# Performance work log

Hardware: AMD Instinct MI355X
Metric: run time of the kernel (lower is better)

The kernel has to match this reference:

```python
import jax, jax.numpy as jnp
import numpy as np

EMBED = 1024
HEADS = 16
DK = EMBED // HEADS


def setup_inputs() -> dict:
    key = jax.random.key(0)
    ks = jax.random.split(key, 6)
    B, S = 2, 2048
    scale = 1.0 / np.sqrt(EMBED)
    x = jax.random.normal(ks[0], (B, S, EMBED), dtype=jnp.float32)
    Wq = jax.random.normal(ks[1], (EMBED, EMBED), dtype=jnp.float32) * scale
    Wk = jax.random.normal(ks[2], (EMBED, EMBED), dtype=jnp.float32) * scale
    Wv = jax.random.normal(ks[3], (EMBED, EMBED), dtype=jnp.float32) * scale
    Wo = jax.random.normal(ks[4], (EMBED, EMBED), dtype=jnp.float32) * scale
    qw = jnp.zeros((HEADS, 1), dtype=jnp.float32)  # quantum_weight, init quantum_scale=0
    return {"x": x, "Wq": Wq, "Wk": Wk, "Wv": Wv, "Wo": Wo, "qw": qw}


def reference(x, Wq, Wk, Wv, Wo, qw):
    B, S, E = x.shape
    # nn.Linear with no bias: y = x @ W.T; split heads -> [B,H,S,Dk]
    def proj(W):
        return (x @ W.T).reshape(B, S, HEADS, DK).transpose(0, 2, 1, 3)
    q, k, v = proj(Wq), proj(Wk), proj(Wv)
    scores = jnp.einsum('bhsd,bhtd->bhst', q, k) / np.sqrt(DK)
    attn = jax.nn.softmax(scores, axis=-1)  # dropout in eval mode: identity
    classical = jnp.einsum('bhst,bhtd->bhsd', attn, v)
    w = jax.nn.sigmoid(qw)[:, :, None]  # [H,1,1] per-head mixing weight
    out = w * jnp.sin(classical) + (1.0 - w) * classical
    out = out.transpose(0, 2, 1, 3).reshape(B, S, E)
    return out @ Wo.T
```

## Files before the change

### kernel.cpp

```cpp
#include <hip/hip_runtime.h>
#include <math.h>

constexpr int Ec  = 1024;
constexpr int Hc  = 16;
constexpr int DKc = 64;
constexpr int Bc  = 2;
constexpr int Sc  = 2048;
constexpr int Mc  = Bc * Sc;

typedef _Float16 half8 __attribute__((ext_vector_type(8)));
typedef _Float16 half4 __attribute__((ext_vector_type(4)));
typedef float    floatx4 __attribute__((ext_vector_type(4)));

#define MFMA16(a, b, c) __builtin_amdgcn_mfma_f32_16x16x32_f16(a, b, c, 0, 0, 0)

__device__ __forceinline__ void async_lds16(const _Float16* g, _Float16* l)
{
    __builtin_amdgcn_global_load_lds(
        (const __attribute__((address_space(1))) unsigned int*)g,
        (__attribute__((address_space(3))) unsigned int*)l, 16, 0, 0);
}

__global__ __launch_bounds__(256)
void convert_to_h(const float4* __restrict__ x,
                  const float4* __restrict__ wq,
                  const float4* __restrict__ wk,
                  const float4* __restrict__ wv,
                  const float4* __restrict__ wo,
                  half4* __restrict__ dst)
{
    const int i = blockIdx.x * 256 + threadIdx.x;
    const float4* src; int off;
    if      (i < 1048576) { src = x;  off = i; }
    else if (i < 1310720) { src = wq; off = i - 1048576; }
    else if (i < 1572864) { src = wk; off = i - 1310720; }
    else if (i < 1835008) { src = wv; off = i - 1572864; }
    else                  { src = wo; off = i - 1835008; }
    const float4 v = src[off];
    half4 o;
    o.x = (_Float16)v.x; o.y = (_Float16)v.y;
    o.z = (_Float16)v.z; o.w = (_Float16)v.w;
    dst[i] = o;
}

__device__ __forceinline__ void mfma_gemm_core64(const _Float16* __restrict__ A,
                                                 const _Float16* __restrict__ Bw,
                                                 int m0, int n0,
                                                 _Float16* As, _Float16* Bs,
                                                 floatx4 acc[4][4])
{
    const int tid  = threadIdx.x;
    const int wave = tid >> 6, lane = tid & 63;
    const int l16  = lane & 15, quad = lane >> 4;
    const int wrow = (wave >> 1) * 64, wcol = (wave & 1) * 64;

    const int srow8  = lane >> 3;
    const int schunk = (lane & 7) ^ (srow8 & 7);
    const _Float16* ga = A  + (size_t)(m0 + wave * 32 + srow8) * Ec + schunk * 8;
    const _Float16* gb = Bw + (size_t)(n0 + wave * 32 + srow8) * Ec + schunk * 8;
    _Float16* lA = As + (size_t)(wave * 32) * 64;
    _Float16* lB = Bs + (size_t)(wave * 32) * 64;

    for (int kt = 0; kt < Ec; kt += 64) {
#pragma unroll
        for (int c = 0; c < 4; ++c) {
            async_lds16(ga + (size_t)(c * 8) * Ec + kt, lA + c * 512);
            async_lds16(gb + (size_t)(c * 8) * Ec + kt, lB + c * 512);
        }
        __syncthreads();

        half8 af[4][2], bf[4][2];
#pragma unroll
        for (int i = 0; i < 4; ++i) {
            const int ra = wrow + i * 16 + l16;
            const int rb = wcol + i * 16 + l16;
#pragma unroll
            for (int kc = 0; kc < 2; ++kc) {
                af[i][kc] = *(const half8*)&As[ra * 64 + (((quad + kc * 4) ^ (ra & 7)) * 8)];
                bf[i][kc] = *(const half8*)&Bs[rb * 64 + (((quad + kc * 4) ^ (rb & 7)) * 8)];
            }
        }
#pragma unroll
        for (int i = 0; i < 4; ++i)
#pragma unroll
            for (int j = 0; j < 4; ++j) {
                acc[i][j] = MFMA16(af[i][0], bf[j][0], acc[i][j]);
                acc[i][j] = MFMA16(af[i][1], bf[j][1], acc[i][j]);
            }
        __syncthreads();
    }
}

__global__ __launch_bounds__(256)
void gemm_qkv_mfma(const _Float16* __restrict__ xh,
                   const _Float16* __restrict__ wqh,
                   const _Float16* __restrict__ wkh,
                   const _Float16* __restrict__ wvh,
                   _Float16* __restrict__ Qh,
                   _Float16* __restrict__ Kh,
                   _Float16* __restrict__ VTh)
{
    __shared__ __align__(16) _Float16 As[128 * 64];
    __shared__ __align__(16) _Float16 Bs[128 * 64];
    const int z = blockIdx.z;
    const _Float16* W = (z == 0) ? wqh : (z == 1) ? wkh : wvh;
    const int m0 = blockIdx.y * 128, n0 = blockIdx.x * 128;

    floatx4 acc[4][4] = {};
    mfma_gemm_core64(xh, W, m0, n0, As, Bs, acc);

    const int tid  = threadIdx.x;
    const int wave = tid >> 6, lane = tid & 63;
    const int l16  = lane & 15, quad = lane >> 4;
    const int wrow = (wave >> 1) * 64, wcol = (wave & 1) * 64;

    if (z == 2) {
#pragma unroll
        for (int i = 0; i < 4; ++i)
#pragma unroll
            for (int j = 0; j < 4; ++j) {
                const int n  = n0 + wcol + j * 16 + l16;
                const int hh = n >> 6, d = n & 63;
                const int mb = m0 + wrow + i * 16 + quad * 4;
                const int bb = mb >> 11, s = mb & (Sc - 1);
                half4 pk;
#pragma unroll
                for (int r = 0; r < 4; ++r) pk[r] = (_Float16)acc[i][j][r];
                *(half4*)&VTh[((size_t)((bb * Hc + hh) * DKc + d)) * Sc + s] = pk;
            }
    } else {
        _Float16* out = (z == 0) ? Qh : Kh;
        const float scale = (z == 0) ? 0.125f : 1.0f;
#pragma unroll
        for (int i = 0; i < 4; ++i)
#pragma unroll
            for (int j = 0; j < 4; ++j) {
                const int n = n0 + wcol + j * 16 + l16;
#pragma unroll
                for (int r = 0; r < 4; ++r) {
                    const int m = m0 + wrow + i * 16 + quad * 4 + r;
                    out[(size_t)m * Ec + n] = (_Float16)(acc[i][j][r] * scale);
                }
            }
    }
}

__global__ __launch_bounds__(256)
void gemm_out_mfma(const _Float16* __restrict__ A,
                   const _Float16* __restrict__ W,
                   float* __restrict__ C)
{
    __shared__ __align__(16) _Float16 As[128 * 64];
    __shared__ __align__(16) _Float16 Bs[64 * 64];
    const int m0 = blockIdx.y * 128, n0 = blockIdx.x * 64;

    const int tid  = threadIdx.x;
    const int wave = tid >> 6, lane = tid & 63;
    const int l16  = lane & 15, quad = lane >> 4;
    const int wrow = (wave >> 1) * 64, wcol = (wave & 1) * 32;

    const int srow8  = lane >> 3;
    const int schunk = (lane & 7) ^ (srow8 & 7);
    const _Float16* ga = A + (size_t)(m0 + wave * 32 + srow8) * Ec + schunk * 8;
    const _Float16* gb = W + (size_t)(n0 + wave * 16 + srow8) * Ec + schunk * 8;
    _Float16* lA = As + (size_t)(wave * 32) * 64;
    _Float16* lB = Bs + (size_t)(wave * 16) * 64;

    floatx4 acc[4][2] = {};

    for (int kt = 0; kt < Ec; kt += 64) {
#pragma unroll
        for (int c = 0; c < 4; ++c)
            async_lds16(ga + (size_t)(c * 8) * Ec + kt, lA + c * 512);
#pragma unroll
        for (int c = 0; c < 2; ++c)
            async_lds16(gb + (size_t)(c * 8) * Ec + kt, lB + c * 512);
        __syncthreads();

        half8 af[4][2], bf[2][2];
#pragma unroll
        for (int i = 0; i < 4; ++i) {
            const int ra = wrow + i * 16 + l16;
#pragma unroll
            for (int kc = 0; kc < 2; ++kc)
                af[i][kc] = *(const half8*)&As[ra * 64 + (((quad + kc * 4) ^ (ra & 7)) * 8)];
        }
#pragma unroll
        for (int j = 0; j < 2; ++j) {
            const int rb = wcol + j * 16 + l16;
#pragma unroll
            for (int kc = 0; kc < 2; ++kc)
                bf[j][kc] = *(const half8*)&Bs[rb * 64 + (((quad + kc * 4) ^ (rb & 7)) * 8)];
        }
#pragma unroll
        for (int i = 0; i < 4; ++i)
#pragma unroll
            for (int j = 0; j < 2; ++j) {
                acc[i][j] = MFMA16(af[i][0], bf[j][0], acc[i][j]);
                acc[i][j] = MFMA16(af[i][1], bf[j][1], acc[i][j]);
            }
        __syncthreads();
    }

#pragma unroll
    for (int i = 0; i < 4; ++i)
#pragma unroll
        for (int j = 0; j < 2; ++j) {
            const int n = n0 + wcol + j * 16 + l16;
#pragma unroll
            for (int r = 0; r < 4; ++r) {
                const int m = m0 + wrow + i * 16 + quad * 4 + r;
                C[(size_t)m * Ec + n] = acc[i][j][r];
            }
        }
}

__global__ __launch_bounds__(256)
void flash_attn(const _Float16* __restrict__ Qh,
                const _Float16* __restrict__ Kh,
                const _Float16* __restrict__ VTh,
                const float* __restrict__ qw,
                _Float16* __restrict__ Mixh)
{
    constexpr int BM = 128, BN = 64, LDH = 72;
    __shared__ _Float16 Kt[BN][LDH];
    __shared__ _Float16 Vt[DKc][LDH];
    __shared__ _Float16 Ps[BM][LDH];

    const int tid  = threadIdx.x;
    const int wave = tid >> 6, lane = tid & 63;
    const int quad = lane >> 4, l16 = lane & 15;
    const int q0 = blockIdx.x * BM;
    const int bh = blockIdx.y;
    const int h  = bh & (Hc - 1), b = bh >> 4;

    half8 aq[2][2];
#pragma unroll
    for (int u = 0; u < 2; ++u) {
        const _Float16* qp = Qh + (size_t)(b * Sc + q0 + wave * 32 + u * 16 + l16) * Ec
                                + h * DKc + quad * 8;
        aq[u][0] = *(const half8*)qp;
        aq[u][1] = *(const half8*)(qp + 32);
    }

    const int srow = tid >> 2;
    const int sseg = (tid & 3) * 16;
    const _Float16* Kg = Kh + (size_t)(b * Sc + srow) * Ec + h * DKc + sseg;
    const _Float16* Vg = VTh + ((size_t)(bh * DKc + srow)) * Sc + sseg;

    half8 kr0 = *(const half8*)Kg, kr1 = *(const half8*)(Kg + 8);
    half8 vr0 = *(const half8*)Vg, vr1 = *(const half8*)(Vg + 8);
    Kg += (size_t)BN * Ec; Vg += BN;
    *(half8*)&Kt[srow][sseg]     = kr0;
    *(half8*)&Kt[srow][sseg + 8] = kr1;

    floatx4 o[2][4] = {};
    float l_run[2] = {0.f, 0.f};

    for (int n = 0; n < Sc / BN; ++n) {
        __syncthreads();
        *(half8*)&Vt[srow][sseg]     = vr0;
        *(half8*)&Vt[srow][sseg + 8] = vr1;
        const bool more = (n + 1 < Sc / BN);
        if (more) {
            kr0 = *(const half8*)Kg; kr1 = *(const half8*)(Kg + 8);
            vr0 = *(const half8*)Vg; vr1 = *(const half8*)(Vg + 8);
            Kg += (size_t)BN * Ec; Vg += BN;
        }

        floatx4 st[2][4];
#pragma unroll
        for (int i = 0; i < 4; ++i) {
            const half8 ak0 = *(const half8*)&Kt[i * 16 + l16][quad * 8];
            const half8 ak1 = *(const half8*)&Kt[i * 16 + l16][32 + quad * 8];
            const floatx4 z = {0.f, 0.f, 0.f, 0.f};
            st[0][i] = MFMA16(ak1, aq[0][1], MFMA16(ak0, aq[0][0], z));
            st[1][i] = MFMA16(ak1, aq[1][1], MFMA16(ak0, aq[1][0], z));
        }

#pragma unroll
        for (int u = 0; u < 2; ++u) {
            const int prow = wave * 32 + u * 16 + l16;
#pragma unroll
            for (int i = 0; i < 4; ++i) {
                const float p0 = __expf(st[u][i][0]);
                const float p1 = __expf(st[u][i][1]);
                const float p2 = __expf(st[u][i][2]);
                const float p3 = __expf(st[u][i][3]);
                l_run[u] += (p0 + p1) + (p2 + p3);
                half4 pk;
                pk.x = (_Float16)p0; pk.y = (_Float16)p1;
                pk.z = (_Float16)p2; pk.w = (_Float16)p3;
                *(half4*)&Ps[prow][i * 16 + quad * 4] = pk;
            }
        }
        __syncthreads();

        half8 ap[2][2];
#pragma unroll
        for (int u = 0; u < 2; ++u) {
            const _Float16* pp = &Ps[wave * 32 + u * 16 + l16][quad * 8];
            ap[u][0] = *(const half8*)pp;
            ap[u][1] = *(const half8*)(pp + 32);
        }
#pragma unroll
        for (int jd = 0; jd < 4; ++jd) {
            const half8 bv0 = *(const half8*)&Vt[jd * 16 + l16][quad * 8];
            const half8 bv1 = *(const half8*)&Vt[jd * 16 + l16][32 + quad * 8];
#pragma unroll
            for (int u = 0; u < 2; ++u) {
                o[u][jd] = MFMA16(ap[u][0], bv0, o[u][jd]);
                o[u][jd] = MFMA16(ap[u][1], bv1, o[u][jd]);
            }
        }

        if (more) {
            *(half8*)&Kt[srow][sseg]     = kr0;
            *(half8*)&Kt[srow][sseg + 8] = kr1;
        }
    }

    const float wmix = 1.f / (1.f + __expf(-qw[h]));
#pragma unroll
    for (int u = 0; u < 2; ++u) {
        l_run[u] += __shfl_xor(l_run[u], 16);
        l_run[u] += __shfl_xor(l_run[u], 32);
    }
#pragma unroll
    for (int u = 0; u < 2; ++u)
#pragma unroll
        for (int r = 0; r < 4; ++r) {
            const float l = __shfl(l_run[u], (lane & 48) | (quad * 4 + r));
            const float inv = 1.f / l;
            const int m = q0 + wave * 32 + u * 16 + quad * 4 + r;
            _Float16* mp = Mixh + (size_t)(b * Sc + m) * Ec + h * DKc;
#pragma unroll
            for (int jd = 0; jd < 4; ++jd) {
                const float v = o[u][jd][r] * inv;
                mp[jd * 16 + l16] = (_Float16)(wmix * __sinf(v) + (1.f - wmix) * v);
            }
        }
}

extern "C" void kernel_launch(void* const* d_in, const int* in_sizes, int n_in,
                              void* d_out, int out_size, void* d_ws, size_t ws_size,
                              hipStream_t stream)
{
    const float* x  = (const float*)d_in[0];
    const float* Wq = (const float*)d_in[1];
    const float* Wk = (const float*)d_in[2];
    const float* Wv = (const float*)d_in[3];
    const float* Wo = (const float*)d_in[4];
    const float* qw = (const float*)d_in[5];
    float* out = (float*)d_out;

    _Float16* hb   = (_Float16*)d_ws;
    _Float16* xh   = hb;
    _Float16* wqh  = hb + (size_t)4 * 1024 * 1024;
    _Float16* wkh  = hb + (size_t)5 * 1024 * 1024;
    _Float16* wvh  = hb + (size_t)6 * 1024 * 1024;
    _Float16* woh  = hb + (size_t)7 * 1024 * 1024;
    _Float16* Qh   = hb + (size_t)8 * 1024 * 1024;
    _Float16* Kh   = hb + (size_t)12 * 1024 * 1024;
    _Float16* VTh  = hb + (size_t)16 * 1024 * 1024;
    _Float16* mixh = hb + (size_t)20 * 1024 * 1024;

    convert_to_h<<<dim3(8192), dim3(256), 0, stream>>>(
        (const float4*)x, (const float4*)Wq, (const float4*)Wk,
        (const float4*)Wv, (const float4*)Wo, (half4*)hb);

    gemm_qkv_mfma<<<dim3(Ec / 128, Mc / 128, 3), dim3(256), 0, stream>>>(
        xh, wqh, wkh, wvh, Qh, Kh, VTh);

    flash_attn<<<dim3(Sc / 128, Bc * Hc), dim3(256), 0, stream>>>(
        Qh, Kh, VTh, qw, mixh);

    gemm_out_mfma<<<dim3(Ec / 64, Mc / 128), dim3(256), 0, stream>>>(
        mixh, woh, out);
}
```

Measured before the change: 194.9 us.

## Split flash attention KV sequence across two wave groups and merge in LDS

Doubles the flash attention block to 512 threads, with each half of the block processing half of the key/value sequence for the same query tile. Partial sums and output accumulators are combined through shared memory at the end. It also folds log2(e) into the Q scale so the kernel can use the native exp2, and packs P to fp16 with cvt_pkrtz. This raises per-block parallelism and latency hiding, at the cost of more LDS, an extra reduction step, and round-toward-zero fp16 conversion.

```diff
diff --git a/kernel.cpp b/kernel.cpp
--- a/kernel.cpp
+++ b/kernel.cpp
@@ -130,7 +130,7 @@
             }
     } else {
         _Float16* out = (z == 0) ? Qh : Kh;
-        const float scale = (z == 0) ? 0.125f : 1.0f;
+        const float scale = (z == 0) ? 0.18033688011112042f : 1.0f;
 #pragma unroll
         for (int i = 0; i < 4; ++i)
 #pragma unroll
@@ -215,7 +215,7 @@
         }
 }
 
-__global__ __launch_bounds__(256)
+__global__ __launch_bounds__(512)
 void flash_attn(const _Float16* __restrict__ Qh,
                 const _Float16* __restrict__ Kh,
                 const _Float16* __restrict__ VTh,
@@ -223,30 +223,38 @@
                 _Float16* __restrict__ Mixh)
 {
     constexpr int BM = 128, BN = 64, LDH = 72;
-    __shared__ _Float16 Kt[BN][LDH];
-    __shared__ _Float16 Vt[DKc][LDH];
-    __shared__ _Float16 Ps[BM][LDH];
+    constexpr int NT = (Sc / BN) / 2;
+    __shared__ __align__(16) _Float16 KVs[2][2][BN][LDH];
+    __shared__ __align__(16) _Float16 Ps[2][BM][LDH];
+    __shared__ float Ls[BM];
 
     const int tid  = threadIdx.x;
-    const int wave = tid >> 6, lane = tid & 63;
+    const int g    = tid >> 8;
+    const int wl   = (tid >> 6) & 3;
+    const int lane = tid & 63;
     const int quad = lane >> 4, l16 = lane & 15;
     const int q0 = blockIdx.x * BM;
     const int bh = blockIdx.y;
     const int h  = bh & (Hc - 1), b = bh >> 4;
 
+    _Float16 (*Kt)[LDH] = KVs[g][0];
+    _Float16 (*Vt)[LDH] = KVs[g][1];
+    _Float16 (*Pt)[LDH] = Ps[g];
+
     half8 aq[2][2];
 #pragma unroll
     for (int u = 0; u < 2; ++u) {
-        const _Float16* qp = Qh + (size_t)(b * Sc + q0 + wave * 32 + u * 16 + l16) * Ec
+        const _Float16* qp = Qh + (size_t)(b * Sc + q0 + wl * 32 + u * 16 + l16) * Ec
                                 + h * DKc + quad * 8;
         aq[u][0] = *(const half8*)qp;
         aq[u][1] = *(const half8*)(qp + 32);
     }
 
-    const int srow = tid >> 2;
-    const int sseg = (tid & 3) * 16;
-    const _Float16* Kg = Kh + (size_t)(b * Sc + srow) * Ec + h * DKc + sseg;
-    const _Float16* Vg = VTh + ((size_t)(bh * DKc + srow)) * Sc + sseg;
+    const int tl   = tid & 255;
+    const int srow = tl >> 2;
+    const int sseg = (tl & 3) * 16;
+    const _Float16* Kg = Kh + (size_t)(b * Sc + g * (Sc / 2) + srow) * Ec + h * DKc + sseg;
+    const _Float16* Vg = VTh + ((size_t)(bh * DKc + srow)) * Sc + g * (Sc / 2) + sseg;
 
     half8 kr0 = *(const half8*)Kg, kr1 = *(const half8*)(Kg + 8);
     half8 vr0 = *(const half8*)Vg, vr1 = *(const half8*)(Vg + 8);
@@ -257,11 +265,11 @@
     floatx4 o[2][4] = {};
     float l_run[2] = {0.f, 0.f};
 
-    for (int n = 0; n < Sc / BN; ++n) {
+    for (int n = 0; n < NT; ++n) {
         __syncthreads();
         *(half8*)&Vt[srow][sseg]     = vr0;
         *(half8*)&Vt[srow][sseg + 8] = vr1;
-        const bool more = (n + 1 < Sc / BN);
+        const bool more = (n + 1 < NT);
         if (more) {
             kr0 = *(const half8*)Kg; kr1 = *(const half8*)(Kg + 8);
             vr0 = *(const half8*)Vg; vr1 = *(const half8*)(Vg + 8);
@@ -280,18 +288,20 @@
 
 #pragma unroll
         for (int u = 0; u < 2; ++u) {
-            const int prow = wave * 32 + u * 16 + l16;
+            const int prow = wl * 32 + u * 16 + l16;
 #pragma unroll
             for (int i = 0; i < 4; ++i) {
-                const float p0 = __expf(st[u][i][0]);
-                const float p1 = __expf(st[u][i][1]);
-                const float p2 = __expf(st[u][i][2]);
-                const float p3 = __expf(st[u][i][3]);
+                const float p0 = __builtin_amdgcn_exp2f(st[u][i][0]);
+                const float p1 = __builtin_amdgcn_exp2f(st[u][i][1]);
+                const float p2 = __builtin_amdgcn_exp2f(st[u][i][2]);
+                const float p3 = __builtin_amdgcn_exp2f(st[u][i][3]);
                 l_run[u] += (p0 + p1) + (p2 + p3);
+                auto lo = __builtin_amdgcn_cvt_pkrtz(p0, p1);
+                auto hi = __builtin_amdgcn_cvt_pkrtz(p2, p3);
                 half4 pk;
-                pk.x = (_Float16)p0; pk.y = (_Float16)p1;
-                pk.z = (_Float16)p2; pk.w = (_Float16)p3;
-                *(half4*)&Ps[prow][i * 16 + quad * 4] = pk;
+                pk.x = (_Float16)lo.x; pk.y = (_Float16)lo.y;
+                pk.z = (_Float16)hi.x; pk.w = (_Float16)hi.y;
+                *(half4*)&Pt[prow][i * 16 + quad * 4] = pk;
             }
         }
         __syncthreads();
@@ -299,7 +309,7 @@
         half8 ap[2][2];
 #pragma unroll
         for (int u = 0; u < 2; ++u) {
-            const _Float16* pp = &Ps[wave * 32 + u * 16 + l16][quad * 8];
+            const _Float16* pp = &Pt[wl * 32 + u * 16 + l16][quad * 8];
             ap[u][0] = *(const half8*)pp;
             ap[u][1] = *(const half8*)(pp + 32);
         }
@@ -320,26 +330,44 @@
         }
     }
 
-    const float wmix = 1.f / (1.f + __expf(-qw[h]));
 #pragma unroll
     for (int u = 0; u < 2; ++u) {
         l_run[u] += __shfl_xor(l_run[u], 16);
         l_run[u] += __shfl_xor(l_run[u], 32);
     }
-#pragma unroll
-    for (int u = 0; u < 2; ++u)
-#pragma unroll
-        for (int r = 0; r < 4; ++r) {
-            const float l = __shfl(l_run[u], (lane & 48) | (quad * 4 + r));
-            const float inv = 1.f / l;
-            const int m = q0 + wave * 32 + u * 16 + quad * 4 + r;
-            _Float16* mp = Mixh + (size_t)(b * Sc + m) * Ec + h * DKc;
-#pragma unroll
-            for (int jd = 0; jd < 4; ++jd) {
-                const float v = o[u][jd][r] * inv;
-                mp[jd * 16 + l16] = (_Float16)(wmix * __sinf(v) + (1.f - wmix) * v);
-            }
-        }
+
+    __syncthreads();
+    float* Os = (float*)KVs;
+    if (g == 1) {
+#pragma unroll
+        for (int u = 0; u < 2; ++u) {
+            if (quad == 0) Ls[wl * 32 + u * 16 + l16] = l_run[u];
+#pragma unroll
+            for (int jd = 0; jd < 4; ++jd)
+#pragma unroll
+                for (int r = 0; r < 4; ++r)
+                    Os[(wl * 32 + u * 16 + quad * 4 + r) * 66 + jd * 16 + l16] = o[u][jd][r];
+        }
+    }
+    __syncthreads();
+    if (g == 0) {
+        const float wmix = 1.f / (1.f + __expf(-qw[h]));
+#pragma unroll
+        for (int u = 0; u < 2; ++u)
+#pragma unroll
+            for (int r = 0; r < 4; ++r) {
+                const int ml = wl * 32 + u * 16 + quad * 4 + r;
+                const float l0 = __shfl(l_run[u], (lane & 48) | (quad * 4 + r));
+                const float inv = 1.f / (l0 + Ls[ml]);
+                const int m = q0 + ml;
+                _Float16* mp = Mixh + (size_t)(b * Sc + m) * Ec + h * DKc;
+#pragma unroll
+                for (int jd = 0; jd < 4; ++jd) {
+                    const float v = (o[u][jd][r] + Os[ml * 66 + jd * 16 + l16]) * inv;
+                    mp[jd * 16 + l16] = (_Float16)(wmix * __sinf(v) + (1.f - wmix) * v);
+                }
+            }
+    }
 }
 
 extern "C" void kernel_launch(void* const* d_in, const int* in_sizes, int n_in,
@@ -372,7 +400,7 @@
     gemm_qkv_mfma<<<dim3(Ec / 128, Mc / 128, 3), dim3(256), 0, stream>>>(
         xh, wqh, wkh, wvh, Qh, Kh, VTh);
 
-    flash_attn<<<dim3(Sc / 128, Bc * Hc), dim3(256), 0, stream>>>(
+    flash_attn<<<dim3(Sc / 128, Bc * Hc), dim3(512), 0, stream>>>(
         Qh, Kh, VTh, qw, mixh);
 
     gemm_out_mfma<<<dim3(Ec / 64, Mc / 128), dim3(256), 0, stream>>>(
```

After: 191.1 us. About the same (-1.9%).

## Restructure flash attention with split-KV wave groups, async LDS loads and 32x32 MFMA

Applied to the files above, without the earlier changes.

Rewrites the attention kernel to use 512 threads split into two groups that each process half of the key sequence, then combine partial outputs and row sums through shared memory. K/V tiles are double-buffered via global_load_lds async copies into an XOR-swizzled LDS layout. The P tile stays in registers using permlane32_swap instead of a round trip through shared memory. The kernel switches to 32x32x16 MFMA and exp2 with log2e folded into the Q scale. The aim is to cut LDS traffic and barriers and to hide load latency. In exchange it needs more registers and adds a cross-group reduction.

```diff
diff --git a/kernel.cpp b/kernel.cpp
--- a/kernel.cpp
+++ b/kernel.cpp
@@ -10,15 +10,24 @@
 
 typedef _Float16 half8 __attribute__((ext_vector_type(8)));
 typedef _Float16 half4 __attribute__((ext_vector_type(4)));
-typedef float    floatx4 __attribute__((ext_vector_type(4)));
+typedef float    floatx4  __attribute__((ext_vector_type(4)));
+typedef float    floatx16 __attribute__((ext_vector_type(16)));
+typedef unsigned int uint2v __attribute__((ext_vector_type(2)));
+typedef unsigned int uint4v __attribute__((ext_vector_type(4)));
 
 #define MFMA16(a, b, c) __builtin_amdgcn_mfma_f32_16x16x32_f16(a, b, c, 0, 0, 0)
+#define MFMA32(a, b, c) __builtin_amdgcn_mfma_f32_32x32x16_f16(a, b, c, 0, 0, 0)
 
 __device__ __forceinline__ void async_lds16(const _Float16* g, _Float16* l)
 {
     __builtin_amdgcn_global_load_lds(
         (const __attribute__((address_space(1))) unsigned int*)g,
         (__attribute__((address_space(3))) unsigned int*)l, 16, 0, 0);
+}
+
+__device__ __forceinline__ unsigned pkh2(float a, float b)
+{
+    return __builtin_bit_cast(unsigned, __builtin_amdgcn_cvt_pkrtz(a, b));
 }
 
 __global__ __launch_bounds__(256)
@@ -130,7 +139,7 @@
             }
     } else {
         _Float16* out = (z == 0) ? Qh : Kh;
-        const float scale = (z == 0) ? 0.125f : 1.0f;
+        const float scale = (z == 0) ? 0.18033688011112042f : 1.0f;
 #pragma unroll
         for (int i = 0; i < 4; ++i)
 #pragma unroll
@@ -215,131 +224,140 @@
         }
 }
 
-__global__ __launch_bounds__(256)
+__global__ __launch_bounds__(512, 4)
 void flash_attn(const _Float16* __restrict__ Qh,
                 const _Float16* __restrict__ Kh,
                 const _Float16* __restrict__ VTh,
                 const float* __restrict__ qw,
                 _Float16* __restrict__ Mixh)
 {
-    constexpr int BM = 128, BN = 64, LDH = 72;
-    __shared__ _Float16 Kt[BN][LDH];
-    __shared__ _Float16 Vt[DKc][LDH];
-    __shared__ _Float16 Ps[BM][LDH];
+    constexpr int BM = 128, BN = 64;
+    constexpr int NT = (Sc / BN) / 2;
+    __shared__ __align__(16) _Float16 KV[2][2][2][64 * 64];
+    __shared__ float Ls[2][128];
 
     const int tid  = threadIdx.x;
-    const int wave = tid >> 6, lane = tid & 63;
-    const int quad = lane >> 4, l16 = lane & 15;
+    const int g    = tid >> 8;
+    const int wl   = (tid >> 6) & 3;
+    const int lane = tid & 63;
+    const int l31  = lane & 31, hi = lane >> 5;
     const int q0 = blockIdx.x * BM;
     const int bh = blockIdx.y;
     const int h  = bh & (Hc - 1), b = bh >> 4;
 
-    half8 aq[2][2];
-#pragma unroll
-    for (int u = 0; u < 2; ++u) {
-        const _Float16* qp = Qh + (size_t)(b * Sc + q0 + wave * 32 + u * 16 + l16) * Ec
-                                + h * DKc + quad * 8;
-        aq[u][0] = *(const half8*)qp;
-        aq[u][1] = *(const half8*)(qp + 32);
-    }
-
-    const int srow = tid >> 2;
-    const int sseg = (tid & 3) * 16;
-    const _Float16* Kg = Kh + (size_t)(b * Sc + srow) * Ec + h * DKc + sseg;
-    const _Float16* Vg = VTh + ((size_t)(bh * DKc + srow)) * Sc + sseg;
-
-    half8 kr0 = *(const half8*)Kg, kr1 = *(const half8*)(Kg + 8);
-    half8 vr0 = *(const half8*)Vg, vr1 = *(const half8*)(Vg + 8);
-    Kg += (size_t)BN * Ec; Vg += BN;
-    *(half8*)&Kt[srow][sseg]     = kr0;
-    *(half8*)&Kt[srow][sseg + 8] = kr1;
-
-    floatx4 o[2][4] = {};
-    float l_run[2] = {0.f, 0.f};
-
-    for (int n = 0; n < Sc / BN; ++n) {
-        __syncthreads();
-        *(half8*)&Vt[srow][sseg]     = vr0;
-        *(half8*)&Vt[srow][sseg + 8] = vr1;
-        const bool more = (n + 1 < Sc / BN);
-        if (more) {
-            kr0 = *(const half8*)Kg; kr1 = *(const half8*)(Kg + 8);
-            vr0 = *(const half8*)Vg; vr1 = *(const half8*)(Vg + 8);
-            Kg += (size_t)BN * Ec; Vg += BN;
-        }
-
-        floatx4 st[2][4];
-#pragma unroll
-        for (int i = 0; i < 4; ++i) {
-            const half8 ak0 = *(const half8*)&Kt[i * 16 + l16][quad * 8];
-            const half8 ak1 = *(const half8*)&Kt[i * 16 + l16][32 + quad * 8];
-            const floatx4 z = {0.f, 0.f, 0.f, 0.f};
-            st[0][i] = MFMA16(ak1, aq[0][1], MFMA16(ak0, aq[0][0], z));
-            st[1][i] = MFMA16(ak1, aq[1][1], MFMA16(ak0, aq[1][0], z));
-        }
-
-#pragma unroll
-        for (int u = 0; u < 2; ++u) {
-            const int prow = wave * 32 + u * 16 + l16;
-#pragma unroll
-            for (int i = 0; i < 4; ++i) {
-                const float p0 = __expf(st[u][i][0]);
-                const float p1 = __expf(st[u][i][1]);
-                const float p2 = __expf(st[u][i][2]);
-                const float p3 = __expf(st[u][i][3]);
-                l_run[u] += (p0 + p1) + (p2 + p3);
-                half4 pk;
-                pk.x = (_Float16)p0; pk.y = (_Float16)p1;
-                pk.z = (_Float16)p2; pk.w = (_Float16)p3;
-                *(half4*)&Ps[prow][i * 16 + quad * 4] = pk;
-            }
-        }
-        __syncthreads();
-
-        half8 ap[2][2];
-#pragma unroll
-        for (int u = 0; u < 2; ++u) {
-            const _Float16* pp = &Ps[wave * 32 + u * 16 + l16][quad * 8];
-            ap[u][0] = *(const half8*)pp;
-            ap[u][1] = *(const half8*)(pp + 32);
-        }
-#pragma unroll
-        for (int jd = 0; jd < 4; ++jd) {
-            const half8 bv0 = *(const half8*)&Vt[jd * 16 + l16][quad * 8];
-            const half8 bv1 = *(const half8*)&Vt[jd * 16 + l16][32 + quad * 8];
-#pragma unroll
-            for (int u = 0; u < 2; ++u) {
-                o[u][jd] = MFMA16(ap[u][0], bv0, o[u][jd]);
-                o[u][jd] = MFMA16(ap[u][1], bv1, o[u][jd]);
-            }
-        }
-
-        if (more) {
-            *(half8*)&Kt[srow][sseg]     = kr0;
-            *(half8*)&Kt[srow][sseg + 8] = kr1;
-        }
-    }
-
-    const float wmix = 1.f / (1.f + __expf(-qw[h]));
-#pragma unroll
-    for (int u = 0; u < 2; ++u) {
-        l_run[u] += __shfl_xor(l_run[u], 16);
-        l_run[u] += __shfl_xor(l_run[u], 32);
-    }
-#pragma unroll
-    for (int u = 0; u < 2; ++u)
-#pragma unroll
-        for (int r = 0; r < 4; ++r) {
-            const float l = __shfl(l_run[u], (lane & 48) | (quad * 4 + r));
-            const float inv = 1.f / l;
-            const int m = q0 + wave * 32 + u * 16 + quad * 4 + r;
-            _Float16* mp = Mixh + (size_t)(b * Sc + m) * Ec + h * DKc;
-#pragma unroll
-            for (int jd = 0; jd < 4; ++jd) {
-                const float v = o[u][jd][r] * inv;
-                mp[jd * 16 + l16] = (_Float16)(wmix * __sinf(v) + (1.f - wmix) * v);
-            }
-        }
+    half8 aq[4];
+    {
+        const _Float16* qp = Qh + (size_t)(b * Sc + q0 + wl * 32 + l31) * Ec
+                                + h * DKc + hi * 8;
+#pragma unroll
+        for (int ks = 0; ks < 4; ++ks) aq[ks] = *(const half8*)(qp + ks * 16);
+    }
+
+    const int srow   = lane >> 3;
+    const int schunk = (lane & 7) ^ srow;
+    const _Float16* Kg = Kh + (size_t)(b * Sc + g * (Sc / 2) + wl * 16 + srow) * Ec
+                            + h * DKc + schunk * 8;
+    const _Float16* Vg = VTh + ((size_t)(bh * DKc + wl * 16 + srow)) * Sc
+                             + g * (Sc / 2) + schunk * 8;
+
+    floatx16 o[2] = {};
+    float l_run = 0.f;
+    const int xk = l31 & 7;
+
+    {
+        _Float16* kb = KV[g][0][0] + (wl * 16) * 64;
+        _Float16* vb = KV[g][0][1] + (wl * 16) * 64;
+        async_lds16(Kg, kb);
+        async_lds16(Kg + (size_t)8 * Ec, kb + 8 * 64);
+        async_lds16(Vg, vb);
+        async_lds16(Vg + (size_t)8 * Sc, vb + 8 * 64);
+    }
+    __syncthreads();
+
+    int cur = 0;
+    for (int n = 0; n < NT; ++n) {
+        if (n + 1 < NT) {
+            _Float16* kb = KV[g][cur ^ 1][0] + (wl * 16) * 64;
+            _Float16* vb = KV[g][cur ^ 1][1] + (wl * 16) * 64;
+            const _Float16* kg = Kg + (size_t)(n + 1) * BN * Ec;
+            const _Float16* vg = Vg + (size_t)(n + 1) * BN;
+            async_lds16(kg, kb);
+            async_lds16(kg + (size_t)8 * Ec, kb + 8 * 64);
+            async_lds16(vg, vb);
+            async_lds16(vg + (size_t)8 * Sc, vb + 8 * 64);
+        }
+        const _Float16* Kb = KV[g][cur][0];
+        const _Float16* Vb = KV[g][cur][1];
+
+#pragma unroll
+        for (int t = 0; t < 2; ++t) {
+            floatx16 st = {};
+#pragma unroll
+            for (int ks = 0; ks < 4; ++ks) {
+                const half8 ak = *(const half8*)
+                    (Kb + (t * 32 + l31) * 64 + ((((ks << 1) | hi) ^ xk) << 3));
+                st = MFMA32(ak, aq[ks], st);
+            }
+            float p[16];
+#pragma unroll
+            for (int r = 0; r < 16; ++r) p[r] = __builtin_amdgcn_exp2f(st[r]);
+#pragma unroll
+            for (int r = 0; r < 16; ++r) l_run += p[r];
+            half8 pa[2];
+#pragma unroll
+            for (int e = 0; e < 2; ++e) {
+                const unsigned X0 = pkh2(p[8 * e + 0], p[8 * e + 1]);
+                const unsigned X1 = pkh2(p[8 * e + 2], p[8 * e + 3]);
+                const unsigned Y0 = pkh2(p[8 * e + 4], p[8 * e + 5]);
+                const unsigned Y1 = pkh2(p[8 * e + 6], p[8 * e + 7]);
+                const uint2v s0 = __builtin_amdgcn_permlane32_swap(X0, Y0, false, false);
+                const uint2v s1 = __builtin_amdgcn_permlane32_swap(X1, Y1, false, false);
+                uint4v w;
+                w.x = s0.x; w.y = s1.x; w.z = s0.y; w.w = s1.y;
+                pa[e] = __builtin_bit_cast(half8, w);
+            }
+#pragma unroll
+            for (int dt = 0; dt < 2; ++dt)
+#pragma unroll
+                for (int e = 0; e < 2; ++e) {
+                    const int ks = 2 * t + e;
+                    const half8 bv = *(const half8*)
+                        (Vb + (dt * 32 + l31) * 64 + ((((ks << 1) | hi) ^ xk) << 3));
+                    o[dt] = MFMA32(pa[e], bv, o[dt]);
+                }
+        }
+        __syncthreads();
+        cur ^= 1;
+    }
+
+    l_run += __shfl_xor(l_run, 32);
+    if (hi == 0) Ls[g][wl * 32 + l31] = l_run;
+
+    float* Os = (float*)&KV[0][0][0][0];
+    if (g == 1) {
+#pragma unroll
+        for (int dt = 0; dt < 2; ++dt)
+#pragma unroll
+            for (int r = 0; r < 16; ++r) {
+                const int row = wl * 32 + (r & 3) + 8 * (r >> 2) + 4 * hi;
+                Os[row * 66 + dt * 32 + l31] = o[dt][r];
+            }
+    }
+    __syncthreads();
+    if (g == 0) {
+        const float wmix = 1.f / (1.f + __expf(-qw[h]));
+#pragma unroll
+        for (int r = 0; r < 16; ++r) {
+            const int row = wl * 32 + (r & 3) + 8 * (r >> 2) + 4 * hi;
+            const float inv = 1.f / (Ls[0][row] + Ls[1][row]);
+            _Float16* mp = Mixh + (size_t)(b * Sc + q0 + row) * Ec + h * DKc;
+#pragma unroll
+            for (int dt = 0; dt < 2; ++dt) {
+                const float v = (o[dt][r] + Os[row * 66 + dt * 32 + l31]) * inv;
+                mp[dt * 32 + l31] = (_Float16)(wmix * __sinf(v) + (1.f - wmix) * v);
+            }
+        }
+    }
 }
 
 extern "C" void kernel_launch(void* const* d_in, const int* in_sizes, int n_in,
@@ -372,7 +390,7 @@
     gemm_qkv_mfma<<<dim3(Ec / 128, Mc / 128, 3), dim3(256), 0, stream>>>(
         xh, wqh, wkh, wvh, Qh, Kh, VTh);
 
-    flash_attn<<<dim3(Sc / 128, Bc * Hc), dim3(256), 0, stream>>>(
+    flash_attn<<<dim3(Sc / 128, Bc * Hc), dim3(512), 0, stream>>>(
         Qh, Kh, VTh, qw, mixh);
 
     gemm_out_mfma<<<dim3(Ec / 64, Mc / 128), dim3(256), 0, stream>>>(
```

New measurement: 188.8 us. -3.1%, faster.
